# Kernel tuning notes

Measured on AMD Instinct MI355X. Metric: run time of the kernel, lower is better.

Reference implementation:

```python
import jax, jax.numpy as jnp
import numpy as np

OUT_H = OUT_W = 7
SCALE = 0.25
SR = 2  # sampling_ratio


def setup_inputs() -> dict:
    key = jax.random.key(0)
    k1, k2, k3, k4, k5, k6 = jax.random.split(key, 6)
    B, C, H, W = 2, 256, 200, 304
    N = 1000
    inputs = jax.random.normal(k1, (B, C, H, W), dtype=jnp.float32)
    # rois: (batch_idx, cx, cy, w, h, angle_deg) in IMAGE coords (scale back by 1/SCALE)
    bidx = jax.random.randint(k2, (N,), 0, B).astype(jnp.float32)
    cx = jax.random.uniform(k3, (N,), minval=0.0, maxval=W / SCALE)
    cy = jax.random.uniform(k4, (N,), minval=0.0, maxval=H / SCALE)
    wh = jax.random.uniform(k5, (N, 2), minval=16.0, maxval=256.0)
    ang = jax.random.uniform(k6, (N,), minval=-90.0, maxval=90.0)
    rois = jnp.concatenate([bidx[:, None], cx[:, None], cy[:, None], wh, ang[:, None]], axis=1)
    return {"inputs": inputs, "rois": rois}


def _roi_align_rotated(feats, rois):
    B, C, H, W = feats.shape
    N = rois.shape[0]
    offset = 0.5  # aligned=True continuous-coordinate convention
    bidx = rois[:, 0].astype(jnp.int32)
    cw = rois[:, 1] * SCALE - offset
    ch = rois[:, 2] * SCALE - offset
    rw = rois[:, 3] * SCALE
    rh = rois[:, 4] * SCALE
    theta = rois[:, 5] * (jnp.pi / 180.0)
    cos_t, sin_t = jnp.cos(theta), jnp.sin(theta)

    bin_h = rh / OUT_H
    bin_w = rw / OUT_W
    # fused (bin, subsample) coordinate: t[j] = ph + (iy+0.5)/SR for j = ph*SR+iy
    t_y = (jnp.arange(OUT_H * SR, dtype=feats.dtype) + 0.5) / SR  # [GH]
    t_x = (jnp.arange(OUT_W * SR, dtype=feats.dtype) + 0.5) / SR  # [GW]
    yy = -rh[:, None] / 2.0 + t_y[None, :] * bin_h[:, None]  # [N,GH] roi-local
    xx = -rw[:, None] / 2.0 + t_x[None, :] * bin_w[:, None]  # [N,GW]

    # rotate into feature-map coords
    y = yy[:, :, None] * cos_t[:, None, None] - xx[:, None, :] * sin_t[:, None, None] + ch[:, None, None]
    x = yy[:, :, None] * sin_t[:, None, None] + xx[:, None, :] * cos_t[:, None, None] + cw[:, None, None]

    empty = (y < -1.0) | (y > H) | (x < -1.0) | (x > W)
    y = jnp.clip(y, 0.0, None)
    x = jnp.clip(x, 0.0, None)
    y_low = jnp.clip(jnp.floor(y).astype(jnp.int32), 0, H - 1)
    x_low = jnp.clip(jnp.floor(x).astype(jnp.int32), 0, W - 1)
    y_high = jnp.minimum(y_low + 1, H - 1)
    x_high = jnp.minimum(x_low + 1, W - 1)
    ly = jnp.clip(y - y_low.astype(y.dtype), 0.0, 1.0)
    lx = jnp.clip(x - x_low.astype(x.dtype), 0.0, 1.0)
    hy, hx = 1.0 - ly, 1.0 - lx

    b = bidx[:, None, None]  # [N,1,1] broadcasts with [N,GH,GW] index arrays
    v1 = feats[b, :, y_low, x_low]    # [N,GH,GW,C]
    v2 = feats[b, :, y_low, x_high]
    v3 = feats[b, :, y_high, x_low]
    v4 = feats[b, :, y_high, x_high]

    w1 = (hy * hx)[..., None]
    w2 = (hy * lx)[..., None]
    w3 = (ly * hx)[..., None]
    w4 = (ly * lx)[..., None]
    val = w1 * v1 + w2 * v2 + w3 * v3 + w4 * v4  # [N,GH,GW,C]
    val = jnp.where(empty[..., None], 0.0, val)

    # average the SRxSR samples within each output bin
    val = val.reshape(rois.shape[0], OUT_H, SR, OUT_W, SR, C).mean(axis=(2, 4))
    return jnp.transpose(val, (0, 3, 1, 2))  # [N,C,OUT_H,OUT_W]


def reference(inputs, rois):
    return _roi_align_rotated(inputs, rois)
```

## Files before the change

kernel.cpp:

```cpp
#include <hip/hip_runtime.h>
#include <math.h>

constexpr int Bn = 2, Cn = 256, Hn = 200, Wn = 304, Nroi = 1000;
constexpr int OH = 7, OW = 7, SRn = 2;
constexpr int NS = OH * SRn;
constexpr int NP = NS * NS;
constexpr int NBIN = OH * OW;
constexpr int HWn = Hn * Wn;
constexpr float SCALE = 0.25f;

__device__ __forceinline__ void compute_desc(const float* __restrict__ r, int p,
                                             int& idx, int& dx, int& dyW,
                                             float4& w) {
  float cw = r[1] * SCALE - 0.5f;
  float ch = r[2] * SCALE - 0.5f;
  float rw = r[3] * SCALE;
  float rh = r[4] * SCALE;
  float theta = r[5] * 0.017453292519943295f;
  float cs = cosf(theta), sn = sinf(theta);
  float bin_h = rh * (1.0f / OH);
  float bin_w = rw * (1.0f / OW);
  int ki = p / NS;
  int kj = p - ki * NS;
  float ty = ((float)ki + 0.5f) * (1.0f / SRn);
  float tx = ((float)kj + 0.5f) * (1.0f / SRn);
  float yy = -0.5f * rh + ty * bin_h;
  float xx = -0.5f * rw + tx * bin_w;
  float y = yy * cs - xx * sn + ch;
  float x = yy * sn + xx * cs + cw;
  bool empty = (y < -1.0f) || (y > (float)Hn) || (x < -1.0f) || (x > (float)Wn);
  y = fmaxf(y, 0.0f);
  x = fmaxf(x, 0.0f);
  int yl = min(max((int)floorf(y), 0), Hn - 1);
  int xl = min(max((int)floorf(x), 0), Wn - 1);
  int yh = min(yl + 1, Hn - 1);
  int xh = min(xl + 1, Wn - 1);
  float ly = fminf(fmaxf(y - (float)yl, 0.0f), 1.0f);
  float lx = fminf(fmaxf(x - (float)xl, 0.0f), 1.0f);
  float hy = 1.0f - ly, hx = 1.0f - lx;
  if (empty) {
    w.x = w.y = w.z = w.w = 0.0f;
  } else {
    w.x = hy * hx;
    w.y = hy * lx;
    w.z = ly * hx;
    w.w = ly * lx;
  }
  idx = yl * Wn + xl;
  dx = xh - xl;
  dyW = (yh - yl) * Wn;
}

__device__ __forceinline__ unsigned bf16rne(float f) {
  unsigned u = __float_as_uint(f);
  return (u + 0x7fffu + ((u >> 16) & 1u)) >> 16;
}
__device__ __forceinline__ unsigned bf16pack(float lo, float hi) {
  return bf16rne(lo) | (bf16rne(hi) << 16);
}

__global__ __launch_bounds__(512) void sort_rois(const float* __restrict__ rois,
                                                 int* __restrict__ perm) {
  __shared__ unsigned a[1024];
  int t = threadIdx.x;
  for (int i = t; i < 1024; i += 512) {
    unsigned packed;
    if (i < Nroi) {
      const float* r = rois + (size_t)i * 6;
      int b = (int)r[0];
      int tx = min(max((int)(r[1] * SCALE * (1.0f / 16.0f)), 0), 31);
      int ty = min(max((int)(r[2] * SCALE * (1.0f / 16.0f)), 0), 31);
      unsigned m = 0;
#pragma unroll
      for (int bit = 0; bit < 5; ++bit) {
        m |= (((tx >> bit) & 1u) << (2 * bit)) | (((ty >> bit) & 1u) << (2 * bit + 1));
      }
      unsigned key = ((unsigned)b << 10) | m;
      packed = (key << 10) | (unsigned)i;
    } else {
      packed = 0xFFFFFC00u | (unsigned)i;
    }
    a[i] = packed;
  }
  for (int k = 2; k <= 1024; k <<= 1) {
    for (int j = k >> 1; j > 0; j >>= 1) {
      __syncthreads();
      int i = ((t & ~(j - 1)) << 1) | (t & (j - 1));
      bool up = ((i & k) == 0);
      unsigned x = a[i], y = a[i + j];
      if ((x > y) == up) {
        a[i] = y;
        a[i + j] = x;
      }
    }
  }
  __syncthreads();
  for (int i = t; i < Nroi; i += 512) perm[i] = (int)(a[i] & 1023u);
}

constexpr int TPX = 64, TCH = 64, LP = TPX + 1;
__global__ __launch_bounds__(256) void transpose_bf16(const float* __restrict__ feats,
                                                      unsigned short* __restrict__ ft) {
  __shared__ float tile[TCH * LP];
  int p0 = blockIdx.x * TPX;
  int c0 = blockIdx.y * TCH;
  int b = blockIdx.z;
  int t = threadIdx.x;
  int px4 = t & 15, ch = t >> 4;
#pragma unroll
  for (int i = 0; i < 4; ++i) {
    int c = ch + 16 * i;
    const float4 v = *(const float4*)(feats + ((size_t)b * Cn + c0 + c) * HWn + p0 + px4 * 4);
    tile[c * LP + px4 * 4 + 0] = v.x;
    tile[c * LP + px4 * 4 + 1] = v.y;
    tile[c * LP + px4 * 4 + 2] = v.z;
    tile[c * LP + px4 * 4 + 3] = v.w;
  }
  __syncthreads();
  int o = t & 7;
  int px8 = t >> 3;
#pragma unroll
  for (int pass = 0; pass < 2; ++pass) {
    int p = px8 + 32 * pass;
    uint4 w4;
    w4.x = bf16pack(tile[(o * 8 + 0) * LP + p], tile[(o * 8 + 1) * LP + p]);
    w4.y = bf16pack(tile[(o * 8 + 2) * LP + p], tile[(o * 8 + 3) * LP + p]);
    w4.z = bf16pack(tile[(o * 8 + 4) * LP + p], tile[(o * 8 + 5) * LP + p]);
    w4.w = bf16pack(tile[(o * 8 + 6) * LP + p], tile[(o * 8 + 7) * LP + p]);
    *(uint4*)((char*)ft + (((size_t)b * HWn + p0 + p) * Cn + c0 + o * 8) * 2) = w4;
  }
}

constexpr int HB1 = 25;
__global__ __launch_bounds__(256, 4) void roi_gather8(const unsigned short* __restrict__ ft,
                                                      const float* __restrict__ rois,
                                                      const int* __restrict__ perm,
                                                      float* __restrict__ out) {
  __shared__ int4 s_m[NP];
  __shared__ float4 s_w[NP];
  __shared__ __align__(16) float s_out[Cn * HB1];
  int bid = blockIdx.x;
  int n = perm[((bid & 7) * (Nroi / 8)) + (bid >> 3)];
  const float* r = rois + (size_t)n * 6;
  int t = threadIdx.x;
  if (t < NP) {
    int idx, dx, dy;
    float4 w;
    compute_desc(r, t, idx, dx, dy, w);
    s_m[t] = make_int4(idx * (Cn * 2), dx * (Cn * 2), dy * (Cn * 2), 0);
    s_w[t] = w;
  }
  __syncthreads();
  int b = (int)r[0];
  int lane = t & 63;
  int wv = t >> 6;
  int k = lane & 31;
  int q = lane >> 5;
  const char* fb = (const char*)ft + (size_t)b * HWn * Cn * 2 + (size_t)k * 16;
  float* ob = out + (size_t)n * Cn * NBIN;

#pragma unroll 1
  for (int ph = 0; ph < 2; ++ph) {
    int b0 = ph ? HB1 : 0;
    int b1 = ph ? NBIN : HB1;
    for (int bin = b0 + wv; bin < b1; bin += 4) {
      int bi = bin / OW;
      int bj = bin - bi * OW;
      int p00 = (bi * 2) * NS + bj * 2;
      float acc0 = 0.f, acc1 = 0.f, acc2 = 0.f, acc3 = 0.f;
      float acc4 = 0.f, acc5 = 0.f, acc6 = 0.f, acc7 = 0.f;
#pragma unroll
      for (int s = 0; s < 4; ++s) {
        int p = p00 + (s >> 1) * NS + (s & 1);
        int4 m = s_m[p];
        float4 w = s_w[p];
        const char* A = fb + m.x + q * m.y;
        uint4 vlo = *(const uint4*)(A);
        uint4 vhi = *(const uint4*)(A + m.z);
        float wlo = q ? w.y : w.x;
        float whi = q ? w.w : w.z;
#define ACC(vv, ww)                                                        \
        acc0 += (ww) * __uint_as_float((vv).x << 16);                      \
        acc1 += (ww) * __uint_as_float((vv).x & 0xffff0000u);              \
        acc2 += (ww) * __uint_as_float((vv).y << 16);                      \
        acc3 += (ww) * __uint_as_float((vv).y & 0xffff0000u);              \
        acc4 += (ww) * __uint_as_float((vv).z << 16);                      \
        acc5 += (ww) * __uint_as_float((vv).z & 0xffff0000u);              \
        acc6 += (ww) * __uint_as_float((vv).w << 16);                      \
        acc7 += (ww) * __uint_as_float((vv).w & 0xffff0000u);
        ACC(vlo, wlo)
        ACC(vhi, whi)
#undef ACC
      }
      acc0 += __shfl_xor(acc0, 32);
      acc1 += __shfl_xor(acc1, 32);
      acc2 += __shfl_xor(acc2, 32);
      acc3 += __shfl_xor(acc3, 32);
      acc4 += __shfl_xor(acc4, 32);
      acc5 += __shfl_xor(acc5, 32);
      acc6 += __shfl_xor(acc6, 32);
      acc7 += __shfl_xor(acc7, 32);
      if (q == 0) {
        int col = bin - b0;
        s_out[(k * 8 + 0) * HB1 + col] = acc0 * 0.25f;
        s_out[(k * 8 + 1) * HB1 + col] = acc1 * 0.25f;
        s_out[(k * 8 + 2) * HB1 + col] = acc2 * 0.25f;
        s_out[(k * 8 + 3) * HB1 + col] = acc3 * 0.25f;
        s_out[(k * 8 + 4) * HB1 + col] = acc4 * 0.25f;
        s_out[(k * 8 + 5) * HB1 + col] = acc5 * 0.25f;
        s_out[(k * 8 + 6) * HB1 + col] = acc6 * 0.25f;
        s_out[(k * 8 + 7) * HB1 + col] = acc7 * 0.25f;
      }
    }
    __syncthreads();
    if (ph == 0) {
#pragma unroll
      for (int i2 = 0; i2 < 25; ++i2) {
        int idx = t + 256 * i2;
        int c = idx / 25;
        int bn = idx - c * 25;
        ob[c * NBIN + bn] = s_out[idx];
      }
    } else {
#pragma unroll
      for (int i2 = 0; i2 < 24; ++i2) {
        int idx = t + 256 * i2;
        int c = idx / 24;
        int bn = idx - c * 24;
        ob[c * NBIN + HB1 + bn] = s_out[c * HB1 + bn];
      }
    }
    __syncthreads();
  }
}

__global__ __launch_bounds__(256) void roi_direct(const float* __restrict__ feats,
                                                  const float* __restrict__ rois,
                                                  float* __restrict__ out) {
  __shared__ int s_idx[NP];
  __shared__ int s_dx[NP];
  __shared__ int s_dy[NP];
  __shared__ float4 s_w[NP];
  int n = blockIdx.x;
  const float* r = rois + (size_t)n * 6;
  int t = threadIdx.x;
  if (t < NP) {
    int idx, dx, dy;
    float4 w;
    compute_desc(r, t, idx, dx, dy, w);
    s_idx[t] = idx;
    s_dx[t] = dx;
    s_dy[t] = dy;
    s_w[t] = w;
  }
  __syncthreads();
  int b = (int)r[0];
  const float* f = feats + ((size_t)b * Cn + t) * HWn;
  float* o = out + ((size_t)n * Cn + t) * NBIN;
  for (int bi = 0; bi < OH; ++bi) {
    for (int bj = 0; bj < OW; ++bj) {
      float acc = 0.0f;
#pragma unroll
      for (int s = 0; s < 4; ++s) {
        int p = (bi * 2 + (s >> 1)) * NS + bj * 2 + (s & 1);
        int idx = s_idx[p];
        int dx = s_dx[p];
        int dy = s_dy[p];
        float4 w = s_w[p];
        acc += w.x * f[idx] + w.y * f[idx + dx] + w.z * f[idx + dy] + w.w * f[idx + dy + dx];
      }
      o[bi * OW + bj] = acc * 0.25f;
    }
  }
}

extern "C" void kernel_launch(void* const* d_in, const int* in_sizes, int n_in,
                              void* d_out, int out_size, void* d_ws, size_t ws_size,
                              hipStream_t stream) {
  const float* feats = (const float*)d_in[0];
  const float* rois = (const float*)d_in[1];
  float* out = (float*)d_out;

  size_t ftBytes = (size_t)Bn * HWn * Cn * sizeof(unsigned short);
  size_t need = ftBytes + 4096;
  if (ws_size >= need) {
    unsigned short* ft = (unsigned short*)d_ws;
    int* perm = (int*)((char*)d_ws + ftBytes);
    sort_rois<<<1, 512, 0, stream>>>(rois, perm);
    transpose_bf16<<<dim3(HWn / TPX, Cn / TCH, Bn), 256, 0, stream>>>(feats, ft);
    roi_gather8<<<dim3(Nroi), 256, 0, stream>>>(ft, rois, perm, out);
  } else {
    roi_direct<<<Nroi, 256, 0, stream>>>(feats, rois, out);
  }
}
```

Measured before the change: 281.4 us.

## Use persistent 512-thread blocks looping over sorted ROIs with full-bin staging

Replaces one-block-per-ROI gather with 256 persistent blocks of 512 threads. Each block walks up to four ROIs from its segment of the sorted permutation, so the grid fits in one wave. Output staging now holds all 49 bins in shared memory and writes them contiguously in a single pass, instead of two half passes. This cuts launch and tail effects and simplifies the store loop, but it uses more shared memory per block, lowers occupancy, and serialises ROIs inside each block.

```diff
diff --git a/kernel.cpp b/kernel.cpp
--- a/kernel.cpp
+++ b/kernel.cpp
@@ -131,39 +131,40 @@
   }
 }
 
-constexpr int HB1 = 25;
-__global__ __launch_bounds__(256, 4) void roi_gather8(const unsigned short* __restrict__ ft,
+constexpr int BPX = 32;
+constexpr int SEG = 125;
+__global__ __launch_bounds__(512, 2) void roi_gather9(const unsigned short* __restrict__ ft,
                                                       const float* __restrict__ rois,
                                                       const int* __restrict__ perm,
                                                       float* __restrict__ out) {
   __shared__ int4 s_m[NP];
   __shared__ float4 s_w[NP];
-  __shared__ __align__(16) float s_out[Cn * HB1];
-  int bid = blockIdx.x;
-  int n = perm[((bid & 7) * (Nroi / 8)) + (bid >> 3)];
-  const float* r = rois + (size_t)n * 6;
-  int t = threadIdx.x;
-  if (t < NP) {
-    int idx, dx, dy;
-    float4 w;
-    compute_desc(r, t, idx, dx, dy, w);
-    s_m[t] = make_int4(idx * (Cn * 2), dx * (Cn * 2), dy * (Cn * 2), 0);
-    s_w[t] = w;
-  }
-  __syncthreads();
-  int b = (int)r[0];
+  __shared__ __align__(16) float s_out[Cn * NBIN];
+  int x = blockIdx.x & 7;
+  int jb = blockIdx.x >> 3;
+  int t = threadIdx.x;
   int lane = t & 63;
   int wv = t >> 6;
   int k = lane & 31;
   int q = lane >> 5;
-  const char* fb = (const char*)ft + (size_t)b * HWn * Cn * 2 + (size_t)k * 16;
-  float* ob = out + (size_t)n * Cn * NBIN;
-
-#pragma unroll 1
-  for (int ph = 0; ph < 2; ++ph) {
-    int b0 = ph ? HB1 : 0;
-    int b1 = ph ? NBIN : HB1;
-    for (int bin = b0 + wv; bin < b1; bin += 4) {
+
+  for (int step = 0; step < 4; ++step) {
+    int idxr = step * BPX + jb;
+    if (idxr >= SEG) break;
+    int n = perm[x * SEG + idxr];
+    const float* r = rois + (size_t)n * 6;
+    if (t < NP) {
+      int idx, dx, dy;
+      float4 w;
+      compute_desc(r, t, idx, dx, dy, w);
+      s_m[t] = make_int4(idx * (Cn * 2), dx * (Cn * 2), dy * (Cn * 2), 0);
+      s_w[t] = w;
+    }
+    __syncthreads();
+    int b = (int)r[0];
+    const char* fb = (const char*)ft + (size_t)b * HWn * Cn * 2 + (size_t)k * 16;
+
+    for (int bin = wv; bin < NBIN; bin += 8) {
       int bi = bin / OW;
       int bj = bin - bi * OW;
       int p00 = (bi * 2) * NS + bj * 2;
@@ -201,35 +202,19 @@
       acc6 += __shfl_xor(acc6, 32);
       acc7 += __shfl_xor(acc7, 32);
       if (q == 0) {
-        int col = bin - b0;
-        s_out[(k * 8 + 0) * HB1 + col] = acc0 * 0.25f;
-        s_out[(k * 8 + 1) * HB1 + col] = acc1 * 0.25f;
-        s_out[(k * 8 + 2) * HB1 + col] = acc2 * 0.25f;
-        s_out[(k * 8 + 3) * HB1 + col] = acc3 * 0.25f;
-        s_out[(k * 8 + 4) * HB1 + col] = acc4 * 0.25f;
-        s_out[(k * 8 + 5) * HB1 + col] = acc5 * 0.25f;
-        s_out[(k * 8 + 6) * HB1 + col] = acc6 * 0.25f;
-        s_out[(k * 8 + 7) * HB1 + col] = acc7 * 0.25f;
+        s_out[(k * 8 + 0) * NBIN + bin] = acc0 * 0.25f;
+        s_out[(k * 8 + 1) * NBIN + bin] = acc1 * 0.25f;
+        s_out[(k * 8 + 2) * NBIN + bin] = acc2 * 0.25f;
+        s_out[(k * 8 + 3) * NBIN + bin] = acc3 * 0.25f;
+        s_out[(k * 8 + 4) * NBIN + bin] = acc4 * 0.25f;
+        s_out[(k * 8 + 5) * NBIN + bin] = acc5 * 0.25f;
+        s_out[(k * 8 + 6) * NBIN + bin] = acc6 * 0.25f;
+        s_out[(k * 8 + 7) * NBIN + bin] = acc7 * 0.25f;
       }
     }
     __syncthreads();
-    if (ph == 0) {
-#pragma unroll
-      for (int i2 = 0; i2 < 25; ++i2) {
-        int idx = t + 256 * i2;
-        int c = idx / 25;
-        int bn = idx - c * 25;
-        ob[c * NBIN + bn] = s_out[idx];
-      }
-    } else {
-#pragma unroll
-      for (int i2 = 0; i2 < 24; ++i2) {
-        int idx = t + 256 * i2;
-        int c = idx / 24;
-        int bn = idx - c * 24;
-        ob[c * NBIN + HB1 + bn] = s_out[c * HB1 + bn];
-      }
-    }
+    float* ob = out + (size_t)n * Cn * NBIN;
+    for (int i = t; i < Cn * NBIN; i += 512) ob[i] = s_out[i];
     __syncthreads();
   }
 }
@@ -288,7 +273,7 @@
     int* perm = (int*)((char*)d_ws + ftBytes);
     sort_rois<<<1, 512, 0, stream>>>(rois, perm);
     transpose_bf16<<<dim3(HWn / TPX, Cn / TCH, Bn), 256, 0, stream>>>(feats, ft);
-    roi_gather8<<<dim3(Nroi), 256, 0, stream>>>(ft, rois, perm, out);
+    roi_gather9<<<dim3(8 * BPX), 512, 0, stream>>>(ft, rois, perm, out);
   } else {
     roi_direct<<<Nroi, 256, 0, stream>>>(feats, rois, out);
   }
```

New measurement: 244.8 us. 13.0% less time.
